# Optimization experiments

Measured on AMD Instinct MI355X. Metric: run time of the kernel, lower is better.

Reference implementation:

```python
import jax, jax.numpy as jnp
import numpy as np

B, T = 4, 512
N_CH, N_CLASSES, L = 64, 10, 2
D_MODEL = 769          # 3*256 conv channels + 1 pe channel
D_STATE, D_CONV = 64, 4
D_INNER = 2 * D_MODEL  # expand=2 -> 1538
DT_RANK = 49           # ceil(769/16)


def conv1d(x, w, b, pad, groups=1):
    # x: (B,C,T), w: (O, C//groups, K)
    y = jax.lax.conv_general_dilated(x, w, (1,), pad,
                                     dimension_numbers=('NCH', 'OIH', 'NCH'),
                                     feature_group_count=groups)
    return y + b[None, :, None]


def rmsnorm(x, w, eps=1e-6):
    return x * jax.lax.rsqrt(jnp.mean(x * x, -1, keepdims=True) + eps) * w


def layernorm(x, w, b, eps=1e-5):
    mu = jnp.mean(x, -1, keepdims=True)
    var = jnp.mean((x - mu) ** 2, -1, keepdims=True)
    return (x - mu) * jax.lax.rsqrt(var + eps) * w + b


def mamba(u, Wi, cw, cb, Wx, Wdt, bdt, A_log, Dv, Wo):
    # u: (B,T,D_MODEL)
    xz = u @ Wi.T                                  # (B,T,2*D_INNER)
    xin, z = jnp.split(xz, 2, axis=-1)
    # causal depthwise conv, kernel D_CONV
    xc = conv1d(jnp.swapaxes(xin, 1, 2), cw, cb, [(D_CONV - 1, 0)], groups=D_INNER)
    xin = jax.nn.silu(jnp.swapaxes(xc, 1, 2))      # (B,T,D_INNER)
    dbc = xin @ Wx.T                               # (B,T,DT_RANK+2*D_STATE)
    dt = jax.nn.softplus(dbc[..., :DT_RANK] @ Wdt.T + bdt)   # (B,T,D_INNER)
    Bm = dbc[..., DT_RANK:DT_RANK + D_STATE]       # (B,T,N)
    Cm = dbc[..., DT_RANK + D_STATE:]              # (B,T,N)
    A = -jnp.exp(A_log)                            # (D_INNER,N)

    def step(h, inp):
        u_t, d_t, b_t, c_t = inp                   # (B,D_INNER),(B,D_INNER),(B,N),(B,N)
        dA = jnp.exp(d_t[..., None] * A)           # (B,D_INNER,N)
        h = dA * h + (d_t * u_t)[..., None] * b_t[:, None, :]
        return h, jnp.einsum('bdn,bn->bd', h, c_t)

    tm = lambda a: jnp.swapaxes(a, 0, 1)           # time-major
    h0 = jnp.zeros((u.shape[0], D_INNER, D_STATE), u.dtype)
    _, ys = jax.lax.scan(step, h0, (tm(xin), tm(dt), tm(Bm), tm(Cm)))
    y = tm(ys) + xin * Dv
    y = y * jax.nn.silu(z)
    return y @ Wo.T


def _forward(x, pointconv_w, pointconv_b, conv1_w, conv1_b, conv2_w, conv2_b,
             conv3_w, conv3_b, ln_w, ln_b, out_w, out_b, rms_w, in_proj_w,
             dw_w, dw_b, x_proj_w, dt_w, dt_b, A_log, D_skip, out_proj_w):
    pe = x[..., -1:]                               # (B,T,1)
    h = jnp.swapaxes(x[..., :-1], 1, 2)            # (B,64,T)
    h = jax.nn.silu(conv1d(h, pointconv_w, pointconv_b, 'SAME'))  # dropout=eval
    h = jnp.concatenate([conv1d(h, conv1_w, conv1_b, 'SAME'),
                         conv1d(h, conv2_w, conv2_b, 'SAME'),
                         conv1d(h, conv3_w, conv3_b, 'SAME')], axis=1)
    h = jnp.swapaxes(jax.nn.silu(h), 1, 2)         # (B,T,768)
    h = jnp.concatenate([h, pe], axis=-1)          # (B,T,769)
    for i in range(L):
        h = mamba(rmsnorm(h, rms_w[i]), in_proj_w[i], dw_w[i], dw_b[i],
                  x_proj_w[i], dt_w[i], dt_b[i], A_log[i], D_skip[i],
                  out_proj_w[i]) + h
    h = layernorm(h, ln_w, ln_b)
    return h @ out_w.T + out_b                     # (B,T,N_CLASSES)


def setup_inputs() -> dict:
    key = jax.random.key(0)
    ks = iter(jax.random.split(key, 40))
    nrm = lambda shape, s: jax.random.normal(next(ks), shape, jnp.float32) * s
    x_sig = jax.random.normal(next(ks), (B, T, N_CH), jnp.float32)
    pe = jax.random.uniform(next(ks), (B, T, 1), jnp.float32)
    x = jnp.concatenate([x_sig, pe], axis=-1)
    return {
        'x': x,
        'pointconv_w': nrm((128, 64, 1), 0.1), 'pointconv_b': jnp.zeros(128),
        'conv1_w': nrm((256, 128, 3), 0.05), 'conv1_b': jnp.zeros(256),
        'conv2_w': nrm((256, 128, 9), 0.03), 'conv2_b': jnp.zeros(256),
        'conv3_w': nrm((256, 128, 27), 0.02), 'conv3_b': jnp.zeros(256),
        'ln_w': jnp.ones(D_MODEL), 'ln_b': jnp.zeros(D_MODEL),
        'out_w': nrm((N_CLASSES, D_MODEL), 0.02), 'out_b': jnp.zeros(N_CLASSES),
        'rms_w': jnp.ones((L, D_MODEL)),
        'in_proj_w': nrm((L, 2 * D_INNER, D_MODEL), 0.02),
        'dw_w': nrm((L, D_INNER, 1, D_CONV), 0.2), 'dw_b': jnp.zeros((L, D_INNER)),
        'x_proj_w': nrm((L, DT_RANK + 2 * D_STATE, D_INNER), 0.02),
        'dt_w': nrm((L, D_INNER, DT_RANK), 0.1),
        'dt_b': jnp.full((L, D_INNER), -2.0, jnp.float32),
        'A_log': jnp.log(jnp.tile(jnp.arange(1, D_STATE + 1, dtype=jnp.float32), (L, D_INNER, 1))),
        'D_skip': jnp.ones((L, D_INNER)),
        'out_proj_w': nrm((L, D_MODEL, D_INNER), 0.02),
    }


def reference(x, pointconv_w, pointconv_b, conv1_w, conv1_b, conv2_w, conv2_b,
              conv3_w, conv3_b, ln_w, ln_b, out_w, out_b, rms_w, in_proj_w,
              dw_w, dw_b, x_proj_w, dt_w, dt_b, A_log, D_skip, out_proj_w):
    return _forward(x, pointconv_w, pointconv_b, conv1_w, conv1_b, conv2_w,
                    conv2_b, conv3_w, conv3_b, ln_w, ln_b, out_w, out_b, rms_w,
                    in_proj_w, dw_w, dw_b, x_proj_w, dt_w, dt_b, A_log, D_skip,
                    out_proj_w)
```

## Files before the change

### kernel.cpp

```cpp
#include <hip/hip_runtime.h>
#include <hip/hip_bf16.h>
#include <cstdint>
#include <math.h>

#define DEV static __device__ __forceinline__

typedef __attribute__((ext_vector_type(8))) __bf16 bf16x8v;
typedef __attribute__((ext_vector_type(4))) float f32x4;

constexpr int B = 4, T = 512, BT = B * T;
constexpr int D_MODEL = 769, D_INNER = 1538, D2 = 3076;
constexpr int DT_RANK = 49, D_STATE = 64;
constexpr int NCH = 8, CHT = 64;
constexpr int DGRP = (D_INNER + 15) / 16;
constexpr int KP_MODEL = 832;
constexpr int KP_INNER = 1600;
constexpr int KP_DT    = 64;
constexpr int NP_IN  = 3200;
constexpr int NP_X   = 256;
constexpr int NP_DT  = 1664;
constexpr int NP_OUT = 896;
constexpr int KCONV  = 3456;
constexpr int NCONV  = 768;

DEV float fexp2(float x) { return __builtin_amdgcn_exp2f(x); }
DEV float flog2(float x) { return __builtin_amdgcn_logf(x); }
DEV float frcp(float x) { return __builtin_amdgcn_rcpf(x); }
DEV float siluf(float v) { return v * frcp(1.f + fexp2(-1.44269504f * v)); }
DEV float softplusf(float v) {
  return fmaxf(v, 0.f) + 0.69314718f * flog2(1.f + fexp2(-1.44269504f * fabsf(v)));
}

DEV float wredx(float v) {
#pragma unroll
  for (int o = 1; o < 64; o <<= 1) v += __shfl_xor(v, o);
  return v;
}

#define DPPF(v, ctrl) __uint_as_float((uint)__builtin_amdgcn_mov_dpp((int)__float_as_uint(v), (ctrl), 0xf, 0xf, true))
#define SWZF(v, pat) __uint_as_float((uint)__builtin_amdgcn_ds_swizzle((int)__float_as_uint(v), (pat)))

DEV void gload_lds16(const void* g, void* l) {
  __builtin_amdgcn_global_load_lds(
      (const __attribute__((address_space(1))) uint32_t*)(uintptr_t)g,
      (__attribute__((address_space(3))) uint32_t*)(uint32_t)(uintptr_t)l,
      16, 0, 0);
}


__global__ void front_pointconv(const float* __restrict__ x, const float* __restrict__ pw,
                                const float* __restrict__ pb, __hip_bfloat16* __restrict__ hpbf) {
  int t = blockIdx.x, b = blockIdx.y, c = threadIdx.x;
  __shared__ float xs[64];
  if (c < 64) xs[c] = x[((size_t)b * T + t) * 65 + c];
  __syncthreads();
  float acc = pb[c];
  const float4* pwr = (const float4*)(pw + c * 64);
#pragma unroll
  for (int i = 0; i < 16; ++i) {
    float4 w4 = pwr[i];
    acc = fmaf(w4.x, xs[4 * i + 0], acc);
    acc = fmaf(w4.y, xs[4 * i + 1], acc);
    acc = fmaf(w4.z, xs[4 * i + 2], acc);
    acc = fmaf(w4.w, xs[4 * i + 3], acc);
  }
  hpbf[((size_t)b * T + t) * 128 + c] = __float2bfloat16(siluf(acc));
}

__global__ void im2col_front(const __hip_bfloat16* __restrict__ hpbf,
                             __hip_bfloat16* __restrict__ Xim) {
  int idx = blockIdx.x * 256 + threadIdx.x;
  if (idx >= BT * 432) return;
  int row = idx / 432, r = idx - row * 432;
  int j = r >> 4, seg = r & 15;
  int b = row >> 9, t = row & 511;
  int ts = t - 13 + j;
  uint4 v = {0u, 0u, 0u, 0u};
  if (ts >= 0 && ts < T) v = *(const uint4*)(hpbf + ((size_t)(b * T + ts)) * 128 + seg * 8);
  *(uint4*)(Xim + (size_t)row * KCONV + j * 128 + seg * 8) = v;
}

__global__ void build_conv_wb(const float* __restrict__ c1w, const float* __restrict__ c2w,
                              const float* __restrict__ c3w, const float* __restrict__ b1,
                              const float* __restrict__ b2, const float* __restrict__ b3,
                              __hip_bfloat16* __restrict__ Wfr, float* __restrict__ cb) {
  int total = NCONV * KCONV;
  for (int idx = blockIdx.x * 256 + threadIdx.x; idx < total + NCONV; idx += gridDim.x * 256) {
    if (idx < total) {
      int co = idx / KCONV, r = idx - co * KCONV;
      int j = r >> 7, ci = r & 127;
      float v = 0.f;
      if (co < 256) {
        int k = j - 12;
        if (k >= 0 && k < 3) v = c1w[((size_t)co * 128 + ci) * 3 + k];
      } else if (co < 512) {
        int k = j - 9;
        if (k >= 0 && k < 9) v = c2w[((size_t)(co - 256) * 128 + ci) * 9 + k];
      } else {
        v = c3w[((size_t)(co - 512) * 128 + ci) * 27 + j];
      }
      Wfr[idx] = __float2bfloat16(v);
    } else {
      int i = idx - total;
      cb[i] = (i < 256) ? b1[i] : (i < 512) ? b2[i - 256] : b3[i - 512];
    }
  }
}

__global__ void cvt_all(const float* __restrict__ Wi, const float* __restrict__ Wx,
                        const float* __restrict__ Wdt, const float* __restrict__ Wo,
                        __hip_bfloat16* __restrict__ Wibf, __hip_bfloat16* __restrict__ Wxbf,
                        __hip_bfloat16* __restrict__ Wdtbf, __hip_bfloat16* __restrict__ Wobf) {
  int l = blockIdx.y >> 2, t = blockIdx.y & 3;
  const float* src;
  __hip_bfloat16* dst;
  int N, K, Npad, Kpad;
  if (t == 0) { src = Wi + (size_t)l * D2 * D_MODEL; dst = Wibf + (size_t)l * NP_IN * KP_MODEL;
                N = D2; K = D_MODEL; Npad = NP_IN; Kpad = KP_MODEL; }
  else if (t == 1) { src = Wx + (size_t)l * (DT_RANK + 2 * D_STATE) * D_INNER;
                dst = Wxbf + (size_t)l * NP_X * KP_INNER;
                N = DT_RANK + 2 * D_STATE; K = D_INNER; Npad = NP_X; Kpad = KP_INNER; }
  else if (t == 2) { src = Wdt + (size_t)l * D_INNER * DT_RANK; dst = Wdtbf + (size_t)l * NP_DT * KP_DT;
                N = D_INNER; K = DT_RANK; Npad = NP_DT; Kpad = KP_DT; }
  else { src = Wo + (size_t)l * D_MODEL * D_INNER; dst = Wobf + (size_t)l * NP_OUT * KP_INNER;
                N = D_MODEL; K = D_INNER; Npad = NP_OUT; Kpad = KP_INNER; }
  int total = Npad * Kpad;
  for (int idx = blockIdx.x * 256 + threadIdx.x; idx < total; idx += gridDim.x * 256) {
    int n = idx / Kpad, k = idx - n * Kpad;
    float v = (n < N && k < K) ? src[(size_t)n * K + k] : 0.f;
    dst[idx] = __float2bfloat16(v);
  }
}

__global__ void zero_pad_cols(__hip_bfloat16* __restrict__ buf, int rows, int ld, int c0) {
  int w = ld - c0;
  int total = rows * w;
  int idx = blockIdx.x * 256 + threadIdx.x;
  if (idx < total) buf[(size_t)(idx / w) * ld + c0 + (idx % w)] = __float2bfloat16(0.f);
}

template <int EPI>
__global__ __launch_bounds__(256) void gemm_bf16(const __hip_bfloat16* __restrict__ A,
                                                 const __hip_bfloat16* __restrict__ W,
                                                 float* __restrict__ C, int M, int Nreal, int Kp,
                                                 const float* extra, int ldadd, int ldc,
                                                 float2* auxv, __hip_bfloat16* auxb,
                                                 const __hip_bfloat16* auxr) {
  __shared__ __align__(16) __hip_bfloat16 As[128 * 64];
  __shared__ __align__(16) __hip_bfloat16 Bs[128 * 64];
  const int tid = threadIdx.x;
  const int wid = tid >> 6, lane = tid & 63;
  const int wr = wid >> 1, wc = wid & 1;
  const int m0 = blockIdx.y * 128, n0 = blockIdx.x * 128;
  f32x4 acc[4][4] = {};
  const int lrow = lane >> 3;
  const int cbyte = ((lane & 7) << 4) ^ (lrow << 4);
  const char* Ab = (const char*)A;
  const char* Wb = (const char*)W;
  const size_t strideAB = (size_t)Kp * 2;
  const int swz = (lane & 7) << 4;

  int kbeg = 0, kend = Kp;
  if constexpr (EPI == 6) {
    int khalf = (((Kp >> 1) + 63) >> 6) << 6;
    if (blockIdx.z == 0) kend = khalf; else kbeg = khalf;
  }

  for (int k0 = kbeg; k0 < kend; k0 += 64) {
#pragma unroll
    for (int i = 0; i < 4; ++i) {
      int seg = i * 4 + wid;
      int row = seg * 8 + lrow;
      gload_lds16(Ab + (size_t)(m0 + row) * strideAB + k0 * 2 + cbyte, (char*)As + seg * 1024);
      gload_lds16(Wb + (size_t)(n0 + row) * strideAB + k0 * 2 + cbyte, (char*)Bs + seg * 1024);
    }
    __syncthreads();
#pragma unroll
    for (int kk = 0; kk < 2; ++kk) {
      int kb = kk * 64 + ((lane >> 4) << 4);
      bf16x8v af[4], bfr[4];
#pragma unroll
      for (int mi = 0; mi < 4; ++mi) {
        int row = wr * 64 + mi * 16 + (lane & 15);
        af[mi] = *(const bf16x8v*)((const char*)As + row * 128 + (kb ^ swz));
      }
#pragma unroll
      for (int ni = 0; ni < 4; ++ni) {
        int row = wc * 64 + ni * 16 + (lane & 15);
        bfr[ni] = *(const bf16x8v*)((const char*)Bs + row * 128 + (kb ^ swz));
      }
#pragma unroll
      for (int mi = 0; mi < 4; ++mi)
#pragma unroll
        for (int ni = 0; ni < 4; ++ni)
          acc[mi][ni] = __builtin_amdgcn_mfma_f32_16x16x32_bf16(af[mi], bfr[ni], acc[mi][ni], 0, 0, 0);
    }
    __syncthreads();
  }

#pragma unroll
  for (int mi = 0; mi < 4; ++mi) {
#pragma unroll
    for (int ni = 0; ni < 4; ++ni) {
      int n = n0 + wc * 64 + ni * 16 + (lane & 15);
      if (n < Nreal) {
        int mb = m0 + wr * 64 + mi * 16 + ((lane >> 4) << 2);
#pragma unroll
        for (int v = 0; v < 4; ++v) {
          float val = acc[mi][ni][v];
          int m = mb + v;
          if constexpr (EPI == 1) {
            val = softplusf(val + extra[n]);
            float du = __bfloat162float(auxr[(size_t)m * KP_INNER + n]);
            auxv[(size_t)m * D_INNER + n] = make_float2(val, val * du);
          } else if constexpr (EPI == 6) {
            C[((size_t)blockIdx.z * M + m) * ldc + n] = val;
          } else if constexpr (EPI == 7) {
            auxb[(size_t)m * ldc + n] = __float2bfloat16(val);
          } else {
            C[(size_t)m * ldc + n] = val;
          }
        }
      }
    }
  }
}

__global__ __launch_bounds__(256) void combine_conv_rms(const float* __restrict__ p,
                                                        const float* __restrict__ cb,
                                                        const float* __restrict__ x,
                                                        const float* __restrict__ rmsw,
                                                        float* __restrict__ h,
                                                        __hip_bfloat16* __restrict__ ubf) {
  int m = blockIdx.x;
  __shared__ float sh[D_MODEL];
  __shared__ float red[4];
  int wid = threadIdx.x >> 6, lane = threadIdx.x & 63;
  float ss = 0.f;
  for (int n = threadIdx.x; n < D_MODEL; n += 256) {
    float v;
    if (n < NCONV)
      v = siluf(p[(size_t)m * NCONV + n] + p[(size_t)BT * NCONV + (size_t)m * NCONV + n] + cb[n]);
    else
      v = x[(size_t)m * 65 + 64];
    sh[n] = v;
    h[(size_t)m * D_MODEL + n] = v;
    ss = fmaf(v, v, ss);
  }
  ss = wredx(ss);
  if (lane == 0) red[wid] = ss;
  __syncthreads();
  float sc = rsqrtf((red[0] + red[1] + red[2] + red[3]) * (1.f / D_MODEL) + 1e-6f);
  for (int i = threadIdx.x; i < KP_MODEL; i += 256) {
    float v = (i < D_MODEL) ? sh[i] * sc * rmsw[i] : 0.f;
    ubf[(size_t)m * KP_MODEL + i] = __float2bfloat16(v);
  }
}

__global__ __launch_bounds__(256) void combine_out_rms(const float* __restrict__ p,
                                                       const float* __restrict__ rmsw,
                                                       float* __restrict__ h,
                                                       __hip_bfloat16* __restrict__ ubf) {
  int m = blockIdx.x;
  __shared__ float sh[D_MODEL];
  __shared__ float red[4];
  int wid = threadIdx.x >> 6, lane = threadIdx.x & 63;
  float ss = 0.f;
  for (int n = threadIdx.x; n < D_MODEL; n += 256) {
    size_t i = (size_t)m * D_MODEL + n;
    float v = h[i] + p[i] + p[(size_t)BT * D_MODEL + i];
    sh[n] = v;
    h[i] = v;
    ss = fmaf(v, v, ss);
  }
  ss = wredx(ss);
  if (lane == 0) red[wid] = ss;
  __syncthreads();
  float sc = rsqrtf((red[0] + red[1] + red[2] + red[3]) * (1.f / D_MODEL) + 1e-6f);
  for (int i = threadIdx.x; i < KP_MODEL; i += 256) {
    float v = (i < D_MODEL) ? sh[i] * sc * rmsw[i] : 0.f;
    ubf[(size_t)m * KP_MODEL + i] = __float2bfloat16(v);
  }
}

__global__ __launch_bounds__(256) void combine_ln(const float* __restrict__ p,
                                                  const float* __restrict__ h,
                                                  const float* __restrict__ lnw,
                                                  const float* __restrict__ lnb,
                                                  const float* __restrict__ ow,
                                                  const float* __restrict__ ob,
                                                  float* __restrict__ out) {
  int row = blockIdx.x;
  __shared__ float sh[D_MODEL];
  __shared__ float red[4];
  int wid = threadIdx.x >> 6, lane = threadIdx.x & 63;
  float s = 0.f;
  for (int i = threadIdx.x; i < D_MODEL; i += 256) {
    size_t ix = (size_t)row * D_MODEL + i;
    float v = h[ix] + p[ix] + p[(size_t)BT * D_MODEL + ix];
    sh[i] = v;
    s += v;
  }
  s = wredx(s);
  if (lane == 0) red[wid] = s;
  __syncthreads();
  float mean = (red[0] + red[1] + red[2] + red[3]) * (1.f / D_MODEL);
  __syncthreads();
  float vs = 0.f;
  for (int i = threadIdx.x; i < D_MODEL; i += 256) { float dd = sh[i] - mean; vs = fmaf(dd, dd, vs); }
  vs = wredx(vs);
  if (lane == 0) red[wid] = vs;
  __syncthreads();
  float var = (red[0] + red[1] + red[2] + red[3]) * (1.f / D_MODEL);
  float inv = rsqrtf(var + 1e-5f);
  for (int i = threadIdx.x; i < D_MODEL; i += 256)
    sh[i] = (sh[i] - mean) * inv * lnw[i] + lnb[i];
  __syncthreads();
  for (int c = wid; c < 10; c += 4) {
    float acc = 0.f;
    for (int i = lane; i < D_MODEL; i += 64) acc = fmaf(sh[i], ow[(size_t)c * D_MODEL + i], acc);
    acc = wredx(acc);
    if (lane == 0) out[(size_t)row * 10 + c] = acc + ob[c];
  }
}

__global__ void combine_xproj(const float* __restrict__ p, __hip_bfloat16* __restrict__ dtbf,
                              __hip_bfloat16* __restrict__ bcb) {
  int i = blockIdx.x * 256 + threadIdx.x;
  if (i >= BT * 192) return;
  int m = i / 192, n = i - m * 192;
  if (n >= DT_RANK + 2 * D_STATE) return;
  float v = p[(size_t)m * 256 + n] + p[(size_t)(BT + m) * 256 + n];
  if (n < 64) dtbf[(size_t)m * 64 + n] = __float2bfloat16(n < DT_RANK ? v : 0.f);
  if (n >= DT_RANK && n < DT_RANK + D_STATE)
    bcb[((size_t)m * 64 + (n - DT_RANK)) * 2] = __float2bfloat16(v);
  else if (n >= DT_RANK + D_STATE)
    bcb[((size_t)m * 64 + (n - DT_RANK - D_STATE)) * 2 + 1] = __float2bfloat16(v);
}

__global__ void dwconv_silu(const __hip_bfloat16* __restrict__ xz, const float* __restrict__ cw,
                            const float* __restrict__ cb, __hip_bfloat16* __restrict__ xinbf) {
  int idx = blockIdx.x * 256 + threadIdx.x;
  if (idx >= BT * D_INNER) return;
  int bt = idx / D_INNER;
  int d = idx - bt * D_INNER;
  int t = bt & (T - 1);
  float acc = cb[d];
  const __hip_bfloat16* col = xz + (size_t)bt * D2 + d;
#pragma unroll
  for (int k = 0; k < 4; ++k) {
    int tt = t + k - 3;
    float v = (tt >= 0) ? __bfloat162float(col[(ptrdiff_t)(k - 3) * D2]) : 0.f;
    acc = fmaf(cw[d * 4 + k], v, acc);
  }
  acc = siluf(acc);
  xinbf[(size_t)bt * KP_INNER + d] = __float2bfloat16(acc);
}


#define FCOMP2(REG, T0L, T0G)                                                \
  {                                                                          \
    float4 qa0 = *(const float4*)&dtsA[(T0L)];                               \
    float4 qa1 = *(const float4*)&dtsA[(T0L) + 4];                           \
    float4 ua0 = *(const float4*)&dtusA[(T0L)];                              \
    float4 ua1 = *(const float4*)&dtusA[(T0L) + 4];                          \
    float4 qb0 = *(const float4*)&dtsB[(T0L)];                               \
    float4 qb1 = *(const float4*)&dtsB[(T0L) + 4];                           \
    float4 ub0 = *(const float4*)&dtusB[(T0L)];                              \
    float4 ub1 = *(const float4*)&dtusB[(T0L) + 4];                          \
    float dtvA[8] = {qa0.x, qa0.y, qa0.z, qa0.w, qa1.x, qa1.y, qa1.z, qa1.w};\
    float duvA[8] = {ua0.x, ua0.y, ua0.z, ua0.w, ua1.x, ua1.y, ua1.z, ua1.w};\
    float dtvB[8] = {qb0.x, qb0.y, qb0.z, qb0.w, qb1.x, qb1.y, qb1.z, qb1.w};\
    float duvB[8] = {ub0.x, ub0.y, ub0.z, ub0.w, ub1.x, ub1.y, ub1.z, ub1.w};\
    float vvA[8], vvB[8];                                                    \
    _Pragma("unroll") for (int k = 0; k < 8; ++k) {                          \
      float Bv = __uint_as_float(REG[k] << 16);                              \
      float Cv = __uint_as_float(REG[k] & 0xffff0000u);                      \
      hA = fmaf(fexp2(dtvA[k] * a2A), hA, duvA[k] * Bv);                     \
      hB = fmaf(fexp2(dtvB[k] * a2B), hB, duvB[k] * Bv);                     \
      vvA[k] = hA * Cv;                                                      \
      vvB[k] = hB * Cv;                                                      \
    }                                                                        \
    _Pragma("unroll") for (int k = 0; k < 4; ++k) {                          \
      float sA = bb0 ? vvA[k] : vvA[k + 4];                                  \
      float kA = bb0 ? vvA[k + 4] : vvA[k];                                  \
      vvA[k] = kA + DPPF(sA, 0xB1);                                          \
      float sB = bb0 ? vvB[k] : vvB[k + 4];                                  \
      float kB = bb0 ? vvB[k + 4] : vvB[k];                                  \
      vvB[k] = kB + DPPF(sB, 0xB1);                                          \
    }                                                                        \
    _Pragma("unroll") for (int k = 0; k < 2; ++k) {                          \
      float sA = bb1 ? vvA[k] : vvA[k + 2];                                  \
      float kA = bb1 ? vvA[k + 2] : vvA[k];                                  \
      vvA[k] = kA + DPPF(sA, 0x4E);                                          \
      float sB = bb1 ? vvB[k] : vvB[k + 2];                                  \
      float kB = bb1 ? vvB[k + 2] : vvB[k];                                  \
      vvB[k] = kB + DPPF(sB, 0x4E);                                          \
    }                                                                        \
    {                                                                        \
      float sA = bb2 ? vvA[0] : vvA[1];                                      \
      float kA = bb2 ? vvA[1] : vvA[0];                                      \
      vvA[0] = kA + SWZF(sA, 0x101F);                                        \
      float sB = bb2 ? vvB[0] : vvB[1];                                      \
      float kB = bb2 ? vvB[1] : vvB[0];                                      \
      vvB[0] = kB + SWZF(sB, 0x101F);                                        \
    }                                                                        \
    float yA = vvA[0], yB = vvB[0];                                          \
    yA += DPPF(yA, 0x128);  yB += DPPF(yB, 0x128);                           \
    yA += SWZF(yA, 0x401F); yB += SWZF(yB, 0x401F);                          \
    yA += __shfl_xor(yA, 32); yB += __shfl_xor(yB, 32);                      \
    if (lane < 8) {                                                          \
      int trow = ((T0L) + brl) * 17;                                         \
      if (vA) {                                                              \
        float yo = (yA + xinS[trow + 2 * wid] * dskA) * siluf(xzS[trow + 2 * wid]); \
        ybf[(rb + (T0G) + brl) * KP_INNER + dA] = __float2bfloat16(yo);      \
      }                                                                      \
      if (vB) {                                                              \
        float yo = (yB + xinS[trow + 2 * wid + 1] * dskB) * siluf(xzS[trow + 2 * wid + 1]); \
        ybf[(rb + (T0G) + brl) * KP_INNER + dB] = __float2bfloat16(yo);      \
      }                                                                      \
    }                                                                        \
  }

__global__ __launch_bounds__(512) void scan_fused(const uint* __restrict__ bcp16,
                                                  const float2* __restrict__ dtdu,
                                                  const __hip_bfloat16* __restrict__ xinbf,
                                                  const __hip_bfloat16* __restrict__ xzbf,
                                                  const float* __restrict__ A_log,
                                                  const float* __restrict__ Dskip,
                                                  __hip_bfloat16* __restrict__ ybf) {
  __shared__ __align__(16) float dts[2][16 * 68];
  __shared__ __align__(16) float dtus[2][16 * 68];
  __shared__ float xins[2][CHT * 17];
  __shared__ float xzs[2][CHT * 17];
  int tid = threadIdx.x, wid = tid >> 6, lane = tid & 63;
  int dg = blockIdx.x % DGRP, b = blockIdx.x / DGRP;
  int d0 = dg * 16;
  int dA = d0 + wid * 2, dB = dA + 1;
  bool vA = (dA < D_INNER), vB = (dB < D_INNER);
  int dcA = vA ? dA : (D_INNER - 1);
  int dcB = vB ? dB : (D_INNER - 1);
  const size_t rb = (size_t)b * T;

  auto stage = [&](int c, int s) {
#pragma unroll
    for (int j = 0; j < 2; ++j) {
      int t2 = tid + j * 512;
      int stt = t2 >> 4, sdd = t2 & 15;
      float2 dq = dtdu[(rb + c * CHT + stt) * D_INNER + d0 + sdd];
      dts[s][sdd * 68 + stt] = dq.x;
      dtus[s][sdd * 68 + stt] = dq.y;
      xins[s][stt * 17 + sdd] = __bfloat162float(xinbf[(rb + c * CHT + stt) * KP_INNER + d0 + sdd]);
      xzs[s][stt * 17 + sdd] = __bfloat162float(xzbf[(rb + c * CHT + stt) * D2 + D_INNER + d0 + sdd]);
    }
  };

  stage(0, 0);

  const bool bb2 = lane & 4, bb1 = lane & 2, bb0 = lane & 1;
  const int brl = ((lane & 1) << 2) | (lane & 2) | ((lane & 4) >> 2);
  float a2A = -__expf(A_log[(size_t)dcA * D_STATE + lane]) * 1.44269504f;
  float a2B = -__expf(A_log[(size_t)dcB * D_STATE + lane]) * 1.44269504f;
  float dskA = Dskip[dcA], dskB = Dskip[dcB];
  float hA = 0.f, hB = 0.f;
  const uint* bgp = bcp16 + rb * 64 + lane;

  __syncthreads();

  uint bA[8], bB[8];
#pragma unroll
  for (int k = 0; k < 8; ++k) bA[k] = bgp[k * 64];

  for (int ch = 0; ch < NCH; ++ch) {
    int s = ch & 1;
    const float* dtsA = &dts[s][(2 * wid) * 68];
    const float* dtusA = &dtus[s][(2 * wid) * 68];
    const float* dtsB = &dts[s][(2 * wid + 1) * 68];
    const float* dtusB = &dtus[s][(2 * wid + 1) * 68];
    const float* xinS = &xins[s][0];
    const float* xzS = &xzs[s][0];
    if (ch + 1 < NCH) stage(ch + 1, s ^ 1);
    const uint* bp = bgp + (size_t)ch * CHT * 64;
#pragma unroll
    for (int gi = 0; gi < 4; ++gi) {
      int t0l = gi * 16;
      int t0g = ch * CHT + t0l;
#pragma unroll
      for (int k = 0; k < 8; ++k) bB[k] = bp[(t0l + 8 + k) * 64];
      FCOMP2(bA, t0l, t0g);
      if (!(ch == NCH - 1 && gi == 3)) {
#pragma unroll
        for (int k = 0; k < 8; ++k) bA[k] = bp[(t0l + 16 + k) * 64];
      }
      FCOMP2(bB, t0l + 8, t0g + 8);
    }
    __syncthreads();
  }
}

extern "C" void kernel_launch(void* const* d_in, const int* in_sizes, int n_in,
                              void* d_out, int out_size, void* d_ws, size_t ws_size,
                              hipStream_t stream) {
  const float* x    = (const float*)d_in[0];
  const float* pcw  = (const float*)d_in[1];
  const float* pcb  = (const float*)d_in[2];
  const float* c1w  = (const float*)d_in[3];
  const float* c1b  = (const float*)d_in[4];
  const float* c2w  = (const float*)d_in[5];
  const float* c2b  = (const float*)d_in[6];
  const float* c3w  = (const float*)d_in[7];
  const float* c3b  = (const float*)d_in[8];
  const float* lnw  = (const float*)d_in[9];
  const float* lnb  = (const float*)d_in[10];
  const float* ow   = (const float*)d_in[11];
  const float* ob   = (const float*)d_in[12];
  const float* rmsw = (const float*)d_in[13];
  const float* Wi   = (const float*)d_in[14];
  const float* dww  = (const float*)d_in[15];
  const float* dwb  = (const float*)d_in[16];
  const float* Wx   = (const float*)d_in[17];
  const float* Wdt  = (const float*)d_in[18];
  const float* dtbv = (const float*)d_in[19];
  const float* Alog = (const float*)d_in[20];
  const float* Dsk  = (const float*)d_in[21];
  const float* Wo   = (const float*)d_in[22];
  float* out = (float*)d_out;

  char* w = (char*)d_ws;
  auto alloc = [&](size_t n) { char* p = w; w += (n + 255) & ~(size_t)255; return p; };
  constexpr size_t REGION = 26400000;
  char* region = alloc(REGION);
  __hip_bfloat16* hpbf = (__hip_bfloat16*)region;
  __hip_bfloat16* Xim  = (__hip_bfloat16*)(region + 600064);
  __hip_bfloat16* Wfr  = (__hip_bfloat16*)(region + 14755840 + 256);
  float* cb768         = (float*)(region + 20065024);
  float2* dtduT        = (float2*)region;
  __hip_bfloat16* bcbf = (__hip_bfloat16*)(region + 25198592);

  float* hbuf          = (float*)alloc((size_t)BT * D_MODEL * 4);
  __hip_bfloat16* ubf  = (__hip_bfloat16*)alloc((size_t)BT * KP_MODEL * 2);
  __hip_bfloat16* xzbf = (__hip_bfloat16*)alloc((size_t)BT * D2 * 2);
  __hip_bfloat16* xinbf= (__hip_bfloat16*)alloc((size_t)BT * KP_INNER * 2);
  __hip_bfloat16* dtbf = (__hip_bfloat16*)alloc((size_t)BT * KP_DT * 2);
  __hip_bfloat16* ybf  = (__hip_bfloat16*)alloc((size_t)BT * KP_INNER * 2);
  __hip_bfloat16* Wibf = (__hip_bfloat16*)alloc((size_t)2 * NP_IN * KP_MODEL * 2);
  __hip_bfloat16* Wxbf = (__hip_bfloat16*)alloc((size_t)2 * NP_X * KP_INNER * 2);
  __hip_bfloat16* Wdtbf= (__hip_bfloat16*)alloc((size_t)2 * NP_DT * KP_DT * 2);
  __hip_bfloat16* Wobf = (__hip_bfloat16*)alloc((size_t)2 * NP_OUT * KP_INNER * 2);
  float* parts         = (float*)alloc((size_t)2 * BT * D_MODEL * 4);

  front_pointconv<<<dim3(T, B), 128, 0, stream>>>(x, pcw, pcb, hpbf);
  im2col_front<<<(BT * 432) / 256, 256, 0, stream>>>(hpbf, Xim);
  build_conv_wb<<<2048, 256, 0, stream>>>(c1w, c2w, c3w, c1b, c2b, c3b, Wfr, cb768);
  cvt_all<<<dim3(1024, 8), 256, 0, stream>>>(Wi, Wx, Wdt, Wo, Wibf, Wxbf, Wdtbf, Wobf);
  gemm_bf16<6><<<dim3(NCONV / 128, BT / 128, 2), 256, 0, stream>>>(Xim, Wfr, parts, BT, NCONV, KCONV,
                                                                   nullptr, 0, NCONV,
                                                                   nullptr, nullptr, nullptr);
  combine_conv_rms<<<BT, 256, 0, stream>>>(parts, cb768, x, rmsw, hbuf, ubf);
  zero_pad_cols<<<(BT * (KP_INNER - D_INNER) + 255) / 256, 256, 0, stream>>>(xinbf, BT, KP_INNER, D_INNER);
  zero_pad_cols<<<(BT * (KP_INNER - D_INNER) + 255) / 256, 256, 0, stream>>>(ybf, BT, KP_INNER, D_INNER);

  for (int l = 0; l < 2; ++l) {
    const float* Al = Alog + (size_t)l * D_INNER * D_STATE;
    gemm_bf16<7><<<dim3(NP_IN / 128, BT / 128), 256, 0, stream>>>(
        ubf, Wibf + (size_t)l * NP_IN * KP_MODEL, nullptr, BT, D2, KP_MODEL,
        nullptr, 0, D2, nullptr, xzbf, nullptr);
    dwconv_silu<<<(BT * D_INNER + 255) / 256, 256, 0, stream>>>(xzbf, dww + (size_t)l * D_INNER * 4,
                                                                dwb + (size_t)l * D_INNER, xinbf);
    gemm_bf16<6><<<dim3(NP_X / 128, BT / 128, 2), 256, 0, stream>>>(
        xinbf, Wxbf + (size_t)l * NP_X * KP_INNER, parts, BT,
        DT_RANK + 2 * D_STATE, KP_INNER, nullptr, 0, 256, nullptr, nullptr, nullptr);
    combine_xproj<<<(BT * 192 + 255) / 256, 256, 0, stream>>>(parts, dtbf, bcbf);
    gemm_bf16<1><<<dim3(NP_DT / 128, BT / 128), 256, 0, stream>>>(
        dtbf, Wdtbf + (size_t)l * NP_DT * KP_DT, nullptr, BT, D_INNER, KP_DT,
        dtbv + (size_t)l * D_INNER, 0, 0, dtduT, nullptr, xinbf);
    scan_fused<<<dim3(B * DGRP), 512, 0, stream>>>((const uint*)bcbf, dtduT, xinbf, xzbf, Al,
                                                   Dsk + (size_t)l * D_INNER, ybf);
    gemm_bf16<6><<<dim3(NP_OUT / 128, BT / 128, 2), 256, 0, stream>>>(
        ybf, Wobf + (size_t)l * NP_OUT * KP_INNER, parts, BT, D_MODEL, KP_INNER,
        nullptr, 0, D_MODEL, nullptr, nullptr, nullptr);
    if (l == 0) {
      combine_out_rms<<<BT, 256, 0, stream>>>(parts, rmsw + D_MODEL, hbuf, ubf);
    } else {
      combine_ln<<<BT, 256, 0, stream>>>(parts, hbuf, lnw, lnb, ow, ob, out);
    }
  }
}
```

Measured before the change: 499.4 us.

## Replace explicit im2col with halo-padded implicit-GEMM conv and remap GEMM workgroups

The front conv GEMM now reads overlapping row windows directly from a halo-padded activation buffer (stride 256 bytes per time step), replacing the materialized im2col matrix and its kernel. A small kernel zeros the 13-row halos instead. All GEMMs also get a workgroup-ID remap that interleaves tiles in groups of eight, plus the scan loop uses a running pointer for B/C loads. This removes the large im2col write/read traffic and one launch, with the risk of less coalesced overlapping A reads and a remap that may change cache locality.

```diff
diff --git a/kernel.cpp b/kernel.cpp
--- a/kernel.cpp
+++ b/kernel.cpp
@@ -13,6 +13,7 @@
 constexpr int DT_RANK = 49, D_STATE = 64;
 constexpr int NCH = 8, CHT = 64;
 constexpr int DGRP = (D_INNER + 15) / 16;
+constexpr int THALO = 539;
 constexpr int KP_MODEL = 832;
 constexpr int KP_INNER = 1600;
 constexpr int KP_DT    = 64;
@@ -49,7 +50,7 @@
 
 
 __global__ void front_pointconv(const float* __restrict__ x, const float* __restrict__ pw,
-                                const float* __restrict__ pb, __hip_bfloat16* __restrict__ hpbf) {
+                                const float* __restrict__ pb, __hip_bfloat16* __restrict__ hpbfH) {
   int t = blockIdx.x, b = blockIdx.y, c = threadIdx.x;
   __shared__ float xs[64];
   if (c < 64) xs[c] = x[((size_t)b * T + t) * 65 + c];
@@ -64,20 +65,16 @@
     acc = fmaf(w4.z, xs[4 * i + 2], acc);
     acc = fmaf(w4.w, xs[4 * i + 3], acc);
   }
-  hpbf[((size_t)b * T + t) * 128 + c] = __float2bfloat16(siluf(acc));
-}
-
-__global__ void im2col_front(const __hip_bfloat16* __restrict__ hpbf,
-                             __hip_bfloat16* __restrict__ Xim) {
-  int idx = blockIdx.x * 256 + threadIdx.x;
-  if (idx >= BT * 432) return;
-  int row = idx / 432, r = idx - row * 432;
-  int j = r >> 4, seg = r & 15;
-  int b = row >> 9, t = row & 511;
-  int ts = t - 13 + j;
-  uint4 v = {0u, 0u, 0u, 0u};
-  if (ts >= 0 && ts < T) v = *(const uint4*)(hpbf + ((size_t)(b * T + ts)) * 128 + seg * 8);
-  *(uint4*)(Xim + (size_t)row * KCONV + j * 128 + seg * 8) = v;
+  hpbfH[((size_t)b * THALO + 13 + t) * 128 + c] = __float2bfloat16(siluf(acc));
+}
+
+__global__ void zero_halo(__hip_bfloat16* __restrict__ h) {
+  int i = blockIdx.x * 256 + threadIdx.x;
+  if (i >= B * 27 * 128) return;
+  int b = i / (27 * 128), r = i - b * 27 * 128;
+  int row = r >> 7, c = r & 127;
+  int rr = (row < 13) ? row : row + 512;
+  h[((size_t)b * THALO + rr) * 128 + c] = __float2bfloat16(0.f);
 }
 
 __global__ void build_conv_wb(const float* __restrict__ c1w, const float* __restrict__ c2w,
@@ -139,7 +136,7 @@
   if (idx < total) buf[(size_t)(idx / w) * ld + c0 + (idx % w)] = __float2bfloat16(0.f);
 }
 
-template <int EPI>
+template <int EPI, int CONV = 0>
 __global__ __launch_bounds__(256) void gemm_bf16(const __hip_bfloat16* __restrict__ A,
                                                  const __hip_bfloat16* __restrict__ W,
                                                  float* __restrict__ C, int M, int Nreal, int Kp,
@@ -151,13 +148,33 @@
   const int tid = threadIdx.x;
   const int wid = tid >> 6, lane = tid & 63;
   const int wr = wid >> 1, wc = wid & 1;
-  const int m0 = blockIdx.y * 128, n0 = blockIdx.x * 128;
+  int bx = blockIdx.x, by = blockIdx.y;
+  {
+    int gx = gridDim.x, gy = gridDim.y;
+    int nwg = gx * gy;
+    if ((nwg & 7) == 0) {
+      int hid = by * gx + bx;
+      int wkl = (hid & 7) * (nwg >> 3) + (hid >> 3);
+      bx = wkl / gy;
+      by = wkl - bx * gy;
+    }
+  }
+  const int m0 = by * 128, n0 = bx * 128;
   f32x4 acc[4][4] = {};
   const int lrow = lane >> 3;
   const int cbyte = ((lane & 7) << 4) ^ (lrow << 4);
-  const char* Ab = (const char*)A;
   const char* Wb = (const char*)W;
-  const size_t strideAB = (size_t)Kp * 2;
+  const size_t strideB = (size_t)Kp * 2;
+  const char* ArowBase;
+  size_t sA;
+  if constexpr (CONV) {
+    int brow = m0 >> 9;
+    ArowBase = (const char*)A + (size_t)(brow * THALO + (m0 & 511)) * 256;
+    sA = 256;
+  } else {
+    ArowBase = (const char*)A + (size_t)m0 * strideB;
+    sA = strideB;
+  }
   const int swz = (lane & 7) << 4;
 
   int kbeg = 0, kend = Kp;
@@ -171,8 +188,8 @@
     for (int i = 0; i < 4; ++i) {
       int seg = i * 4 + wid;
       int row = seg * 8 + lrow;
-      gload_lds16(Ab + (size_t)(m0 + row) * strideAB + k0 * 2 + cbyte, (char*)As + seg * 1024);
-      gload_lds16(Wb + (size_t)(n0 + row) * strideAB + k0 * 2 + cbyte, (char*)Bs + seg * 1024);
+      gload_lds16(ArowBase + (size_t)row * sA + k0 * 2 + cbyte, (char*)As + seg * 1024);
+      gload_lds16(Wb + (size_t)(n0 + row) * strideB + k0 * 2 + cbyte, (char*)Bs + seg * 1024);
     }
     __syncthreads();
 #pragma unroll
@@ -470,6 +487,7 @@
   uint bA[8], bB[8];
 #pragma unroll
   for (int k = 0; k < 8; ++k) bA[k] = bgp[k * 64];
+  const uint* bq = bgp;
 
   for (int ch = 0; ch < NCH; ++ch) {
     int s = ch & 1;
@@ -480,17 +498,17 @@
     const float* xinS = &xins[s][0];
     const float* xzS = &xzs[s][0];
     if (ch + 1 < NCH) stage(ch + 1, s ^ 1);
-    const uint* bp = bgp + (size_t)ch * CHT * 64;
 #pragma unroll
     for (int gi = 0; gi < 4; ++gi) {
       int t0l = gi * 16;
       int t0g = ch * CHT + t0l;
 #pragma unroll
-      for (int k = 0; k < 8; ++k) bB[k] = bp[(t0l + 8 + k) * 64];
+      for (int k = 0; k < 8; ++k) bB[k] = bq[512 + k * 64];
       FCOMP2(bA, t0l, t0g);
+      bq += 1024;
       if (!(ch == NCH - 1 && gi == 3)) {
 #pragma unroll
-        for (int k = 0; k < 8; ++k) bA[k] = bp[(t0l + 16 + k) * 64];
+        for (int k = 0; k < 8; ++k) bA[k] = bq[k * 64];
       }
       FCOMP2(bB, t0l + 8, t0g + 8);
     }
@@ -530,9 +548,8 @@
   auto alloc = [&](size_t n) { char* p = w; w += (n + 255) & ~(size_t)255; return p; };
   constexpr size_t REGION = 26400000;
   char* region = alloc(REGION);
-  __hip_bfloat16* hpbf = (__hip_bfloat16*)region;
-  __hip_bfloat16* Xim  = (__hip_bfloat16*)(region + 600064);
-  __hip_bfloat16* Wfr  = (__hip_bfloat16*)(region + 14755840 + 256);
+  __hip_bfloat16* hpbfH = (__hip_bfloat16*)region;
+  __hip_bfloat16* Wfr  = (__hip_bfloat16*)(region + 14756096);
   float* cb768         = (float*)(region + 20065024);
   float2* dtduT        = (float2*)region;
   __hip_bfloat16* bcbf = (__hip_bfloat16*)(region + 25198592);
@@ -549,13 +566,12 @@
   __hip_bfloat16* Wobf = (__hip_bfloat16*)alloc((size_t)2 * NP_OUT * KP_INNER * 2);
   float* parts         = (float*)alloc((size_t)2 * BT * D_MODEL * 4);
 
-  front_pointconv<<<dim3(T, B), 128, 0, stream>>>(x, pcw, pcb, hpbf);
-  im2col_front<<<(BT * 432) / 256, 256, 0, stream>>>(hpbf, Xim);
+  zero_halo<<<(B * 27 * 128 + 255) / 256, 256, 0, stream>>>(hpbfH);
+  front_pointconv<<<dim3(T, B), 128, 0, stream>>>(x, pcw, pcb, hpbfH);
   build_conv_wb<<<2048, 256, 0, stream>>>(c1w, c2w, c3w, c1b, c2b, c3b, Wfr, cb768);
   cvt_all<<<dim3(1024, 8), 256, 0, stream>>>(Wi, Wx, Wdt, Wo, Wibf, Wxbf, Wdtbf, Wobf);
-  gemm_bf16<6><<<dim3(NCONV / 128, BT / 128, 2), 256, 0, stream>>>(Xim, Wfr, parts, BT, NCONV, KCONV,
-                                                                   nullptr, 0, NCONV,
-                                                                   nullptr, nullptr, nullptr);
+  gemm_bf16<6, 1><<<dim3(NCONV / 128, BT / 128, 2), 256, 0, stream>>>(
+      hpbfH, Wfr, parts, BT, NCONV, KCONV, nullptr, 0, NCONV, nullptr, nullptr, nullptr);
   combine_conv_rms<<<BT, 256, 0, stream>>>(parts, cb768, x, rmsw, hbuf, ubf);
   zero_pad_cols<<<(BT * (KP_INNER - D_INNER) + 255) / 256, 256, 0, stream>>>(xinbf, BT, KP_INNER, D_INNER);
   zero_pad_cols<<<(BT * (KP_INNER - D_INNER) + 255) / 256, 256, 0, stream>>>(ybf, BT, KP_INNER, D_INNER);
```

Result: faster. 489.3 us (-2.0%).
